# Performance work log

Measured on AMD Instinct MI355X. Metric: run time of the kernel, lower is better.

Reference implementation:

```python
import jax, jax.numpy as jnp
import numpy as np

N_NODES = 50000
N_EDGES = 800000


def _norm(deg):
    # DGL: norm = deg^-0.5 with inf (zero-degree) replaced by 0
    return jnp.where(deg > 0, jax.lax.rsqrt(jnp.maximum(deg, 1.0)), 0.0)


def setup_inputs() -> dict:
    key = jax.random.key(0)
    ks = jax.random.split(key, 8)
    x = jax.random.normal(ks[0], (N_NODES, 128), dtype=jnp.float32)
    W1 = jax.random.normal(ks[1], (128, 128), dtype=jnp.float32) * (1.0 / np.sqrt(128))
    b1 = jnp.zeros((128,), dtype=jnp.float32)
    W2 = jax.random.normal(ks[2], (128, 8), dtype=jnp.float32) * (1.0 / np.sqrt(128))
    b2 = jnp.zeros((8,), dtype=jnp.float32)
    src = jax.random.randint(ks[3], (N_EDGES,), 0, N_NODES, dtype=jnp.int32)
    dst = jax.random.randint(ks[4], (N_EDGES,), 0, N_NODES, dtype=jnp.int32)
    graph_ids = jnp.sort(jax.random.randint(ks[5], (N_NODES,), 0, 100, dtype=jnp.int32))
    return {"x": x, "W1": W1, "b1": b1, "W2": W2, "b2": b2,
            "src": src, "dst": dst, "graph_ids": graph_ids, "num_graphs": 100}


def _graph_conv(x, W, b, src, dst, norm_src, norm_dst):
    # GraphConv norm='both': out = D_in^{-1/2} A (D_out^{-1/2} x W) + b
    h = x @ W                                   # [N, F_out]
    msg = h[src] * norm_src[src, None]          # gather + src norm, [E, F_out]
    agg = jax.ops.segment_sum(msg, dst, num_segments=x.shape[0])  # scatter-add
    return agg * norm_dst[:, None] + b


def reference(x, W1, b1, W2, b2, src, dst, graph_ids, num_graphs):
    n = x.shape[0]
    ones_e = jnp.ones((src.shape[0],), dtype=x.dtype)
    deg_out = jax.ops.segment_sum(ones_e, src, num_segments=n)
    deg_in = jax.ops.segment_sum(ones_e, dst, num_segments=n)
    norm_src = _norm(deg_out)
    norm_dst = _norm(deg_in)

    h = _graph_conv(x, W1, b1, src, dst, norm_src, norm_dst)
    h = jax.nn.relu(h)
    h = _graph_conv(h, W2, b2, src, dst, norm_src, norm_dst)

    # dgl.mean_nodes: per-graph mean of node features
    counts = jax.ops.segment_sum(jnp.ones((n,), dtype=x.dtype), graph_ids,
                                 num_segments=num_graphs)
    sums = jax.ops.segment_sum(h, graph_ids, num_segments=num_graphs)
    return sums / jnp.maximum(counts, 1.0)[:, None]
```

## Files before the change

kernel.cpp:

```cpp
#include <hip/hip_runtime.h>

#define F1 128
#define F2 8
#define CAP 64
#define RH 8192
#define ECH 16384
#define BK 32

typedef unsigned short us8 __attribute__((ext_vector_type(8)));

__device__ inline unsigned short f2bf(float f) {
  unsigned u = __float_as_uint(f);
  u += 0x7FFF + ((u >> 16) & 1);
  return (unsigned short)(u >> 16);
}
__device__ inline float bf2f(unsigned short h) {
  return __uint_as_float(((unsigned)h) << 16);
}

__global__ __launch_bounds__(256) void k_hist(const int* __restrict__ src,
                                              const int* __restrict__ dst,
                                              unsigned short* __restrict__ src16,
                                              unsigned short* __restrict__ dst16,
                                              int* __restrict__ partialA,
                                              int* __restrict__ partialB,
                                              int Epad, int E, int N) {
  __shared__ int binsA[RH];
  __shared__ int binsB[RH];
  int range0 = blockIdx.x * RH;
  int c = blockIdx.y;
  int t = threadIdx.x;
  bool writer = (blockIdx.x == 0);
  for (int i = t; i < RH; i += 256) { binsA[i] = 0; binsB[i] = 0; }
  __syncthreads();
  int e0 = c * ECH, e1 = min(e0 + ECH, Epad);
  for (int base = e0 + t * 4; base < e1; base += 1024) {
    int4 a, b;
    if (base + 4 <= E) {
      a = *(const int4*)&src[base];
      b = *(const int4*)&dst[base];
    } else {
      a.x = (base + 0 < E) ? src[base + 0] : -1;
      a.y = (base + 1 < E) ? src[base + 1] : -1;
      a.z = (base + 2 < E) ? src[base + 2] : -1;
      a.w = (base + 3 < E) ? src[base + 3] : -1;
      b.x = (base + 0 < E) ? dst[base + 0] : -1;
      b.y = (base + 1 < E) ? dst[base + 1] : -1;
      b.z = (base + 2 < E) ? dst[base + 2] : -1;
      b.w = (base + 3 < E) ? dst[base + 3] : -1;
    }
    int av[4] = {a.x, a.y, a.z, a.w};
    int bv[4] = {b.x, b.y, b.z, b.w};
#pragma unroll
    for (int j = 0; j < 4; ++j) {
      int sn = av[j] - range0;
      if (av[j] >= 0 && (unsigned)sn < (unsigned)RH) atomicAdd(&binsA[sn], 1);
      int dn = bv[j] - range0;
      if (bv[j] >= 0 && (unsigned)dn < (unsigned)RH) atomicAdd(&binsB[dn], 1);
    }
    if (writer) {
      ushort4 sa, sb;
      sa.x = av[0] >= 0 ? (unsigned short)av[0] : 0xFFFF;
      sa.y = av[1] >= 0 ? (unsigned short)av[1] : 0xFFFF;
      sa.z = av[2] >= 0 ? (unsigned short)av[2] : 0xFFFF;
      sa.w = av[3] >= 0 ? (unsigned short)av[3] : 0xFFFF;
      sb.x = bv[0] >= 0 ? (unsigned short)bv[0] : 0xFFFF;
      sb.y = bv[1] >= 0 ? (unsigned short)bv[1] : 0xFFFF;
      sb.z = bv[2] >= 0 ? (unsigned short)bv[2] : 0xFFFF;
      sb.w = bv[3] >= 0 ? (unsigned short)bv[3] : 0xFFFF;
      *(ushort4*)&src16[base] = sa;
      *(ushort4*)&dst16[base] = sb;
    }
  }
  __syncthreads();
  for (int i = t; i < RH; i += 256) {
    int n = range0 + i;
    if (n < N) {
      partialA[c * N + n] = binsA[i];
      partialB[c * N + n] = binsB[i];
    }
  }
}

__global__ void k_starts(const int* __restrict__ partialA, const int* __restrict__ partialB,
                         int* __restrict__ starts, int* __restrict__ cnt,
                         float* __restrict__ norm_src, float* __restrict__ norm_dst,
                         unsigned short* __restrict__ esrc16,
                         unsigned short* __restrict__ h1n,
                         float* __restrict__ h2n,
                         float* __restrict__ gsum,
                         const int* __restrict__ gids,
                         float* __restrict__ rcnt,
                         int N, int NCH, int NG) {
  int n = blockIdx.x * 256 + threadIdx.x;
  if (n < NG * F2) gsum[n] = 0.f;
  if (n < NG) {
    int g = n;
    int lo = 0, hi = N;
    while (lo < hi) { int m = (lo + hi) >> 1; if (gids[m] < g) lo = m + 1; else hi = m; }
    int lb = lo;
    lo = 0; hi = N;
    while (lo < hi) { int m = (lo + hi) >> 1; if (gids[m] <= g) lo = m + 1; else hi = m; }
    rcnt[g] = 1.f / fmaxf((float)(lo - lb), 1.f);
  }
  if (n < 16) {
    us8 z = {0, 0, 0, 0, 0, 0, 0, 0};
    *(us8*)&h1n[(size_t)N * 128 + n * 8] = z;
  }
  if (n < 8) h2n[(size_t)N * 8 + n] = 0.f;
  if (n < N) {
    int dout = 0;
#pragma unroll 8
    for (int c = 0; c < NCH; ++c) dout += partialA[c * N + n];
    int run = n * CAP;
#pragma unroll 8
    for (int c = 0; c < NCH; ++c) {
      starts[c * N + n] = run;
      run += partialB[c * N + n];
    }
    int din = run - n * CAP;
    int cn = min(din, CAP);
    cnt[n] = cn;
    int cp = (cn + 15) & ~15;
    for (int pos = cn; pos < cp; ++pos) esrc16[n * CAP + pos] = (unsigned short)N;
    norm_src[n] = dout > 0 ? rsqrtf((float)dout) : 0.f;
    norm_dst[n] = din > 0 ? rsqrtf((float)din) : 0.f;
  }
}

__global__ __launch_bounds__(256) void k_scatter(const unsigned short* __restrict__ src16,
                                                 const unsigned short* __restrict__ dst16,
                                                 const int* __restrict__ starts,
                                                 unsigned short* __restrict__ esrc16,
                                                 int Epad, int N, int NCH) {
  __shared__ int cur[RH];
  int range0 = ((int)blockIdx.x / NCH) * RH;
  int c = (int)blockIdx.x % NCH;
  int t = threadIdx.x;
  for (int i = t; i < RH; i += 256) {
    int n = range0 + i;
    cur[i] = (n < N) ? starts[c * N + n] : 0;
  }
  __syncthreads();
  int e0 = c * ECH, e1 = min(e0 + ECH, Epad);
  for (int base = e0 + t * 8; base < e1; base += 2048) {
    us8 a = *(const us8*)&src16[base];
    us8 b = *(const us8*)&dst16[base];
#pragma unroll
    for (int j = 0; j < 8; ++j) {
      int dn = (int)b[j] - range0;
      if ((unsigned)dn < (unsigned)RH) {
        int node = range0 + dn;
        int p = atomicAdd(&cur[dn], 1);
        if (p < (node + 1) * CAP) esrc16[p] = a[j];
      }
    }
  }
}

__global__ __launch_bounds__(256) void k_gemm1(const float* __restrict__ x,
                                               const float* __restrict__ W1,
                                               const float* __restrict__ norm_src,
                                               unsigned short* __restrict__ h1n, int N) {
  __shared__ float xsT[BK][132];
  __shared__ float Wl[BK][132];
  int row0 = blockIdx.x * 128;
  int tid = threadIdx.x;
  int tc = tid & 15;
  int tr = tid >> 4;
  float acc[8][8] = {{0.f}};

  for (int kb = 0; kb < 128; kb += BK) {
    __syncthreads();
#pragma unroll
    for (int it = 0; it < 4; ++it) {
      int i = tid + it * 256;
      int r = i >> 3, kq = i & 7;
      int grow = row0 + r;
      float4 v = make_float4(0.f, 0.f, 0.f, 0.f);
      if (grow < N) v = *(const float4*)&x[(size_t)grow * 128 + kb + kq * 4];
      xsT[kq * 4 + 0][r] = v.x;
      xsT[kq * 4 + 1][r] = v.y;
      xsT[kq * 4 + 2][r] = v.z;
      xsT[kq * 4 + 3][r] = v.w;
    }
#pragma unroll
    for (int it = 0; it < 4; ++it) {
      int i = tid + it * 256;
      int k = i >> 5, c4 = i & 31;
      *(float4*)&Wl[k][c4 * 4] = *(const float4*)&W1[(size_t)(kb + k) * 128 + c4 * 4];
    }
    __syncthreads();
#pragma unroll 2
    for (int k = 0; k < BK; ++k) {
      float4 xa = *(float4*)&xsT[k][tr * 8];
      float4 xb = *(float4*)&xsT[k][tr * 8 + 4];
      float4 wa = *(float4*)&Wl[k][tc * 4];
      float4 wb = *(float4*)&Wl[k][tc * 4 + 64];
      float xs[8] = {xa.x, xa.y, xa.z, xa.w, xb.x, xb.y, xb.z, xb.w};
      float ws[8] = {wa.x, wa.y, wa.z, wa.w, wb.x, wb.y, wb.z, wb.w};
#pragma unroll
      for (int i = 0; i < 8; ++i)
#pragma unroll
        for (int j = 0; j < 8; ++j) acc[i][j] += xs[i] * ws[j];
    }
  }
#pragma unroll
  for (int i = 0; i < 8; ++i) {
    int grow = row0 + tr * 8 + i;
    if (grow < N) {
      float ns = norm_src[grow];
      ushort4 oa, ob;
      oa.x = f2bf(acc[i][0] * ns); oa.y = f2bf(acc[i][1] * ns);
      oa.z = f2bf(acc[i][2] * ns); oa.w = f2bf(acc[i][3] * ns);
      ob.x = f2bf(acc[i][4] * ns); ob.y = f2bf(acc[i][5] * ns);
      ob.z = f2bf(acc[i][6] * ns); ob.w = f2bf(acc[i][7] * ns);
      *(ushort4*)&h1n[(size_t)grow * 128 + tc * 4] = oa;
      *(ushort4*)&h1n[(size_t)grow * 128 + 64 + tc * 4] = ob;
    }
  }
}

__global__ __launch_bounds__(256) void k_agg1f(const unsigned short* __restrict__ h1n,
                                               const int* __restrict__ cnt,
                                               const unsigned short* __restrict__ esrc16,
                                               const float* __restrict__ norm_dst,
                                               const float* __restrict__ norm_src,
                                               const float* __restrict__ b1,
                                               const float* __restrict__ W2,
                                               float* __restrict__ h2n, int N) {
  int tid = threadIdx.x;
  int lane = tid & 63;
  int g = lane >> 4;
  int fl = lane & 15;
  int node = (blockIdx.x * 256 + tid - lane) / 16 + g;
  if (node >= N) return;
  int cp = (cnt[node] + 15) & ~15;
  int i0 = node * CAP;
  float acc[8] = {0.f, 0.f, 0.f, 0.f, 0.f, 0.f, 0.f, 0.f};
  for (int i = 0; i < cp; i += 16) {
#pragma unroll
    for (int t4 = 0; t4 < 16; t4 += 4) {
      ushort4 ss = *(const ushort4*)&esrc16[i0 + i + t4];
      us8 v0 = *(const us8*)&h1n[(size_t)ss.x * 128 + fl * 8];
      us8 v1 = *(const us8*)&h1n[(size_t)ss.y * 128 + fl * 8];
      us8 v2 = *(const us8*)&h1n[(size_t)ss.z * 128 + fl * 8];
      us8 v3 = *(const us8*)&h1n[(size_t)ss.w * 128 + fl * 8];
#pragma unroll
      for (int j = 0; j < 8; ++j)
        acc[j] += (bf2f(v0[j]) + bf2f(v1[j])) + (bf2f(v2[j]) + bf2f(v3[j]));
    }
  }
  float nd = norm_dst[node];
  float4 bb0 = *(const float4*)&b1[fl * 8];
  float4 bb1 = *(const float4*)&b1[fl * 8 + 4];
  float r[8];
  r[0] = fmaxf(acc[0] * nd + bb0.x, 0.f);
  r[1] = fmaxf(acc[1] * nd + bb0.y, 0.f);
  r[2] = fmaxf(acc[2] * nd + bb0.z, 0.f);
  r[3] = fmaxf(acc[3] * nd + bb0.w, 0.f);
  r[4] = fmaxf(acc[4] * nd + bb1.x, 0.f);
  r[5] = fmaxf(acc[5] * nd + bb1.y, 0.f);
  r[6] = fmaxf(acc[6] * nd + bb1.z, 0.f);
  r[7] = fmaxf(acc[7] * nd + bb1.w, 0.f);
  float4 pa = make_float4(0.f, 0.f, 0.f, 0.f);
  float4 pb = make_float4(0.f, 0.f, 0.f, 0.f);
#pragma unroll
  for (int jj = 0; jj < 8; ++jj) {
    float4 wa = *(const float4*)&W2[(fl * 8 + jj) * 8];
    float4 wb = *(const float4*)&W2[(fl * 8 + jj) * 8 + 4];
    pa.x += r[jj] * wa.x; pa.y += r[jj] * wa.y;
    pa.z += r[jj] * wa.z; pa.w += r[jj] * wa.w;
    pb.x += r[jj] * wb.x; pb.y += r[jj] * wb.y;
    pb.z += r[jj] * wb.z; pb.w += r[jj] * wb.w;
  }
#pragma unroll
  for (int d = 8; d >= 1; d >>= 1) {
    pa.x += __shfl_down(pa.x, d); pa.y += __shfl_down(pa.y, d);
    pa.z += __shfl_down(pa.z, d); pa.w += __shfl_down(pa.w, d);
    pb.x += __shfl_down(pb.x, d); pb.y += __shfl_down(pb.y, d);
    pb.z += __shfl_down(pb.z, d); pb.w += __shfl_down(pb.w, d);
  }
  if (fl == 0) {
    float ns = norm_src[node];
    pa.x *= ns; pa.y *= ns; pa.z *= ns; pa.w *= ns;
    pb.x *= ns; pb.y *= ns; pb.z *= ns; pb.w *= ns;
    *(float4*)&h2n[(size_t)node * 8] = pa;
    *(float4*)&h2n[(size_t)node * 8 + 4] = pb;
  }
}

__global__ __launch_bounds__(256) void k_agg2pool(const float* __restrict__ h2n,
                                                  const int* __restrict__ cnt,
                                                  const unsigned short* __restrict__ esrc16,
                                                  const float* __restrict__ norm_dst,
                                                  const float* __restrict__ b2,
                                                  const int* __restrict__ gids,
                                                  float* __restrict__ gsum, int N) {
  __shared__ float bins[16 * 8];
  __shared__ int sg0;
  int tid = threadIdx.x;
  if (tid < 128) bins[tid] = 0.f;
  int base = blockIdx.x * 32;
  if (tid == 0) sg0 = gids[min(base, N - 1)];
  __syncthreads();
  int node = base + (tid >> 3);
  int j = tid & 7;
  if (node < N) {
    int cp = (cnt[node] + 15) & ~15;
    int i0 = node * CAP;
    float acc = 0.f;
    for (int i = 0; i < cp; i += 8) {
      us8 ss = *(const us8*)&esrc16[i0 + i];
      acc += ((h2n[(size_t)ss[0] * 8 + j] + h2n[(size_t)ss[1] * 8 + j]) +
              (h2n[(size_t)ss[2] * 8 + j] + h2n[(size_t)ss[3] * 8 + j])) +
             ((h2n[(size_t)ss[4] * 8 + j] + h2n[(size_t)ss[5] * 8 + j]) +
              (h2n[(size_t)ss[6] * 8 + j] + h2n[(size_t)ss[7] * 8 + j]));
    }
    float r = acc * norm_dst[node] + b2[j];
    int delta = gids[node] - sg0;
    if (delta < 16) atomicAdd(&bins[delta * 8 + j], r);
    else atomicAdd(&gsum[gids[node] * 8 + j], r);
  }
  __syncthreads();
  if (tid < 128) {
    float v = bins[tid];
    if (v != 0.f) atomicAdd(&gsum[(sg0 + (tid >> 3)) * 8 + (tid & 7)], v);
  }
}

__global__ void k_final(const float* __restrict__ gsum, const float* __restrict__ rcnt,
                        float* __restrict__ out, int total) {
  int i = blockIdx.x * 256 + threadIdx.x;
  if (i < total) out[i] = gsum[i] * rcnt[i >> 3];
}

extern "C" void kernel_launch(void* const* d_in, const int* in_sizes, int n_in,
                              void* d_out, int out_size, void* d_ws, size_t ws_size,
                              hipStream_t stream) {
  const float* x  = (const float*)d_in[0];
  const float* W1 = (const float*)d_in[1];
  const float* b1 = (const float*)d_in[2];
  const float* W2 = (const float*)d_in[3];
  const float* b2 = (const float*)d_in[4];
  const int* src  = (const int*)d_in[5];
  const int* dst  = (const int*)d_in[6];
  const int* gids = (const int*)d_in[7];
  int N = in_sizes[0] / F1;
  int E = in_sizes[5];
  int NG = out_size / F2;
  float* out = (float*)d_out;

  int Epad = (E + 2047) & ~2047;
  int NR  = (N + RH - 1) / RH;
  int NCH = (Epad + ECH - 1) / ECH;

  char* p = (char*)d_ws;
  auto alloc = [&](size_t bytes) -> void* {
    void* r = (void*)p;
    p += (bytes + 255) & ~(size_t)255;
    return r;
  };
  float* gsum    = (float*)alloc((size_t)NG * F2 * 4);
  float* rcnt    = (float*)alloc((size_t)NG * 4);
  unsigned short* src16 = (unsigned short*)alloc((size_t)Epad * 2);
  unsigned short* dst16 = (unsigned short*)alloc((size_t)Epad * 2);
  int* cnt       = (int*)alloc((size_t)N * 4);
  float* norm_src = (float*)alloc((size_t)N * 4);
  float* norm_dst = (float*)alloc((size_t)N * 4);
  unsigned short* esrc16 = (unsigned short*)alloc((size_t)N * CAP * 2);
  unsigned short* h1n = (unsigned short*)alloc((size_t)(N + 1) * F1 * 2);
  float* h2n     = (float*)alloc((size_t)(N + 1) * F2 * 4);
  int* partialA  = (int*)alloc((size_t)NCH * N * 4);
  int* partialB  = (int*)alloc((size_t)NCH * N * 4);
  int* starts    = (int*)alloc((size_t)NCH * N * 4);
  (void)ws_size; (void)n_in;

  k_hist<<<dim3(NR, NCH), 256, 0, stream>>>(src, dst, src16, dst16,
                                            partialA, partialB, Epad, E, N);
  k_starts<<<(N + 255) / 256, 256, 0, stream>>>(partialA, partialB, starts, cnt,
                                                norm_src, norm_dst, esrc16, h1n, h2n,
                                                gsum, gids, rcnt, N, NCH, NG);
  k_scatter<<<NR * NCH, 256, 0, stream>>>(src16, dst16, starts, esrc16, Epad, N, NCH);
  k_gemm1<<<(N + 127) / 128, 256, 0, stream>>>(x, W1, norm_src, h1n, N);
  k_agg1f<<<(N + 15) / 16, 256, 0, stream>>>(h1n, cnt, esrc16, norm_dst, norm_src, b1, W2, h2n, N);
  k_agg2pool<<<((N * 8 + 255) / 256), 256, 0, stream>>>(h2n, cnt, esrc16, norm_dst, b2,
                                                        gids, gsum, N);
  k_final<<<(NG * F2 + 255) / 256, 256, 0, stream>>>(gsum, rcnt, out, NG * F2);
}
```

Baseline: 224.4 us.

## Use split-bf16 MFMA for first GEMM and fold mean scaling into pooling

Replaces the fp32 FMA register-tiled GEMM with bf16 MFMA 16x16x32 instructions. Accuracy is kept by splitting x and W1 into high and low bf16 parts and doing three products per tile. W1 is pre-split and transposed inside k_starts, and x is split on the fly while being staged into shared memory. Separately, the per-graph reciprocal count is applied inside the pooling atomics and the accumulation goes straight into out, which removes the k_final launch and the gsum buffer. The trade-offs are three MFMAs per tile, extra conversion work, and scalar 2-byte output stores in place of vectorized ones.

```diff
diff --git a/kernel.cpp b/kernel.cpp
--- a/kernel.cpp
+++ b/kernel.cpp
@@ -5,9 +5,10 @@
 #define CAP 64
 #define RH 8192
 #define ECH 16384
-#define BK 32
 
 typedef unsigned short us8 __attribute__((ext_vector_type(8)));
+typedef short b16x8 __attribute__((ext_vector_type(8)));
+typedef float f32x4 __attribute__((ext_vector_type(4)));
 
 __device__ inline unsigned short f2bf(float f) {
   unsigned u = __float_as_uint(f);
@@ -88,12 +89,15 @@
                          unsigned short* __restrict__ esrc16,
                          unsigned short* __restrict__ h1n,
                          float* __restrict__ h2n,
-                         float* __restrict__ gsum,
+                         float* __restrict__ out,
                          const int* __restrict__ gids,
                          float* __restrict__ rcnt,
+                         const float* __restrict__ W1,
+                         unsigned short* __restrict__ Wth,
+                         unsigned short* __restrict__ Wtl,
                          int N, int NCH, int NG) {
   int n = blockIdx.x * 256 + threadIdx.x;
-  if (n < NG * F2) gsum[n] = 0.f;
+  if (n < NG * F2) out[n] = 0.f;
   if (n < NG) {
     int g = n;
     int lo = 0, hi = N;
@@ -102,6 +106,14 @@
     lo = 0; hi = N;
     while (lo < hi) { int m = (lo + hi) >> 1; if (gids[m] <= g) lo = m + 1; else hi = m; }
     rcnt[g] = 1.f / fmaxf((float)(lo - lb), 1.f);
+  }
+  if (n < F1 * F1) {
+    int k = n >> 7, cc = n & 127;
+    float v = W1[n];
+    unsigned short hi = f2bf(v);
+    unsigned short lo = f2bf(v - bf2f(hi));
+    Wth[cc * 128 + k] = hi;
+    Wtl[cc * 128 + k] = lo;
   }
   if (n < 16) {
     us8 z = {0, 0, 0, 0, 0, 0, 0, 0};
@@ -159,64 +171,78 @@
 }
 
 __global__ __launch_bounds__(256) void k_gemm1(const float* __restrict__ x,
-                                               const float* __restrict__ W1,
+                                               const unsigned short* __restrict__ Wth,
+                                               const unsigned short* __restrict__ Wtl,
                                                const float* __restrict__ norm_src,
                                                unsigned short* __restrict__ h1n, int N) {
-  __shared__ float xsT[BK][132];
-  __shared__ float Wl[BK][132];
-  int row0 = blockIdx.x * 128;
+  __shared__ unsigned short xh[64][72], xl[64][72];
+  __shared__ unsigned short wh[128][72], wl[128][72];
   int tid = threadIdx.x;
-  int tc = tid & 15;
-  int tr = tid >> 4;
-  float acc[8][8] = {{0.f}};
-
-  for (int kb = 0; kb < 128; kb += BK) {
+  int row0 = blockIdx.x * 64;
+  int L = tid & 63;
+  int wave = tid >> 6;
+  int q = L >> 4, mloc = L & 15;
+  int m0 = wave * 16;
+  f32x4 acc[8];
+#pragma unroll
+  for (int t = 0; t < 8; ++t) acc[t] = (f32x4){0.f, 0.f, 0.f, 0.f};
+
+  for (int kb = 0; kb < 2; ++kb) {
     __syncthreads();
 #pragma unroll
     for (int it = 0; it < 4; ++it) {
-      int i = tid + it * 256;
-      int r = i >> 3, kq = i & 7;
+      int flat = tid + it * 256;
+      int n = flat >> 3, kg = (flat & 7) * 8;
+      us8 vh = *(const us8*)&Wth[n * 128 + kb * 64 + kg];
+      us8 vl = *(const us8*)&Wtl[n * 128 + kb * 64 + kg];
+      *(us8*)&wh[n][kg] = vh;
+      *(us8*)&wl[n][kg] = vl;
+    }
+#pragma unroll
+    for (int it = 0; it < 4; ++it) {
+      int idx = tid + it * 256;
+      int r = idx >> 4, kk = (idx & 15) * 4;
       int grow = row0 + r;
       float4 v = make_float4(0.f, 0.f, 0.f, 0.f);
-      if (grow < N) v = *(const float4*)&x[(size_t)grow * 128 + kb + kq * 4];
-      xsT[kq * 4 + 0][r] = v.x;
-      xsT[kq * 4 + 1][r] = v.y;
-      xsT[kq * 4 + 2][r] = v.z;
-      xsT[kq * 4 + 3][r] = v.w;
-    }
-#pragma unroll
-    for (int it = 0; it < 4; ++it) {
-      int i = tid + it * 256;
-      int k = i >> 5, c4 = i & 31;
-      *(float4*)&Wl[k][c4 * 4] = *(const float4*)&W1[(size_t)(kb + k) * 128 + c4 * 4];
+      if (grow < N) v = *(const float4*)&x[(size_t)grow * 128 + kb * 64 + kk];
+      ushort4 h, l;
+      h.x = f2bf(v.x); l.x = f2bf(v.x - bf2f(h.x));
+      h.y = f2bf(v.y); l.y = f2bf(v.y - bf2f(h.y));
+      h.z = f2bf(v.z); l.z = f2bf(v.z - bf2f(h.z));
+      h.w = f2bf(v.w); l.w = f2bf(v.w - bf2f(h.w));
+      *(ushort4*)&xh[r][kk] = h;
+      *(ushort4*)&xl[r][kk] = l;
     }
     __syncthreads();
-#pragma unroll 2
-    for (int k = 0; k < BK; ++k) {
-      float4 xa = *(float4*)&xsT[k][tr * 8];
-      float4 xb = *(float4*)&xsT[k][tr * 8 + 4];
-      float4 wa = *(float4*)&Wl[k][tc * 4];
-      float4 wb = *(float4*)&Wl[k][tc * 4 + 64];
-      float xs[8] = {xa.x, xa.y, xa.z, xa.w, xb.x, xb.y, xb.z, xb.w};
-      float ws[8] = {wa.x, wa.y, wa.z, wa.w, wb.x, wb.y, wb.z, wb.w};
-#pragma unroll
-      for (int i = 0; i < 8; ++i)
-#pragma unroll
-        for (int j = 0; j < 8; ++j) acc[i][j] += xs[i] * ws[j];
-    }
-  }
-#pragma unroll
-  for (int i = 0; i < 8; ++i) {
-    int grow = row0 + tr * 8 + i;
-    if (grow < N) {
-      float ns = norm_src[grow];
-      ushort4 oa, ob;
-      oa.x = f2bf(acc[i][0] * ns); oa.y = f2bf(acc[i][1] * ns);
-      oa.z = f2bf(acc[i][2] * ns); oa.w = f2bf(acc[i][3] * ns);
-      ob.x = f2bf(acc[i][4] * ns); ob.y = f2bf(acc[i][5] * ns);
-      ob.z = f2bf(acc[i][6] * ns); ob.w = f2bf(acc[i][7] * ns);
-      *(ushort4*)&h1n[(size_t)grow * 128 + tc * 4] = oa;
-      *(ushort4*)&h1n[(size_t)grow * 128 + 64 + tc * 4] = ob;
+#pragma unroll
+    for (int ks = 0; ks < 2; ++ks) {
+      int koff = ks * 32 + q * 8;
+      b16x8 ah = *(const b16x8*)&xh[m0 + mloc][koff];
+      b16x8 al = *(const b16x8*)&xl[m0 + mloc][koff];
+#pragma unroll
+      for (int t = 0; t < 8; ++t) {
+        b16x8 bh = *(const b16x8*)&wh[t * 16 + mloc][koff];
+        b16x8 bl = *(const b16x8*)&wl[t * 16 + mloc][koff];
+        acc[t] = __builtin_amdgcn_mfma_f32_16x16x32_bf16(ah, bh, acc[t], 0, 0, 0);
+        acc[t] = __builtin_amdgcn_mfma_f32_16x16x32_bf16(ah, bl, acc[t], 0, 0, 0);
+        acc[t] = __builtin_amdgcn_mfma_f32_16x16x32_bf16(al, bh, acc[t], 0, 0, 0);
+      }
+    }
+  }
+  int rows[4];
+  float ns[4];
+#pragma unroll
+  for (int reg = 0; reg < 4; ++reg) {
+    rows[reg] = row0 + m0 + q * 4 + reg;
+    ns[reg] = (rows[reg] < N) ? norm_src[rows[reg]] : 0.f;
+  }
+#pragma unroll
+  for (int t = 0; t < 8; ++t) {
+    int col = t * 16 + mloc;
+#pragma unroll
+    for (int reg = 0; reg < 4; ++reg) {
+      if (rows[reg] < N)
+        h1n[(size_t)rows[reg] * 128 + col] = f2bf(acc[t][reg] * ns[reg]);
     }
   }
 }
@@ -296,7 +322,8 @@
                                                   const float* __restrict__ norm_dst,
                                                   const float* __restrict__ b2,
                                                   const int* __restrict__ gids,
-                                                  float* __restrict__ gsum, int N) {
+                                                  const float* __restrict__ rcnt,
+                                                  float* __restrict__ out, int N) {
   __shared__ float bins[16 * 8];
   __shared__ int sg0;
   int tid = threadIdx.x;
@@ -318,21 +345,19 @@
               (h2n[(size_t)ss[6] * 8 + j] + h2n[(size_t)ss[7] * 8 + j]));
     }
     float r = acc * norm_dst[node] + b2[j];
-    int delta = gids[node] - sg0;
+    int gid = gids[node];
+    int delta = gid - sg0;
     if (delta < 16) atomicAdd(&bins[delta * 8 + j], r);
-    else atomicAdd(&gsum[gids[node] * 8 + j], r);
+    else atomicAdd(&out[gid * 8 + j], r * rcnt[gid]);
   }
   __syncthreads();
   if (tid < 128) {
     float v = bins[tid];
-    if (v != 0.f) atomicAdd(&gsum[(sg0 + (tid >> 3)) * 8 + (tid & 7)], v);
-  }
-}
-
-__global__ void k_final(const float* __restrict__ gsum, const float* __restrict__ rcnt,
-                        float* __restrict__ out, int total) {
-  int i = blockIdx.x * 256 + threadIdx.x;
-  if (i < total) out[i] = gsum[i] * rcnt[i >> 3];
+    if (v != 0.f) {
+      int gq = sg0 + (tid >> 3);
+      atomicAdd(&out[gq * 8 + (tid & 7)], v * rcnt[gq]);
+    }
+  }
 }
 
 extern "C" void kernel_launch(void* const* d_in, const int* in_sizes, int n_in,
@@ -361,7 +386,6 @@
     p += (bytes + 255) & ~(size_t)255;
     return r;
   };
-  float* gsum    = (float*)alloc((size_t)NG * F2 * 4);
   float* rcnt    = (float*)alloc((size_t)NG * 4);
   unsigned short* src16 = (unsigned short*)alloc((size_t)Epad * 2);
   unsigned short* dst16 = (unsigned short*)alloc((size_t)Epad * 2);
@@ -371,6 +395,8 @@
   unsigned short* esrc16 = (unsigned short*)alloc((size_t)N * CAP * 2);
   unsigned short* h1n = (unsigned short*)alloc((size_t)(N + 1) * F1 * 2);
   float* h2n     = (float*)alloc((size_t)(N + 1) * F2 * 4);
+  unsigned short* Wth = (unsigned short*)alloc((size_t)F1 * F1 * 2);
+  unsigned short* Wtl = (unsigned short*)alloc((size_t)F1 * F1 * 2);
   int* partialA  = (int*)alloc((size_t)NCH * N * 4);
   int* partialB  = (int*)alloc((size_t)NCH * N * 4);
   int* starts    = (int*)alloc((size_t)NCH * N * 4);
@@ -380,11 +406,10 @@
                                             partialA, partialB, Epad, E, N);
   k_starts<<<(N + 255) / 256, 256, 0, stream>>>(partialA, partialB, starts, cnt,
                                                 norm_src, norm_dst, esrc16, h1n, h2n,
-                                                gsum, gids, rcnt, N, NCH, NG);
+                                                out, gids, rcnt, W1, Wth, Wtl, N, NCH, NG);
   k_scatter<<<NR * NCH, 256, 0, stream>>>(src16, dst16, starts, esrc16, Epad, N, NCH);
-  k_gemm1<<<(N + 127) / 128, 256, 0, stream>>>(x, W1, norm_src, h1n, N);
+  k_gemm1<<<(N + 63) / 64, 256, 0, stream>>>(x, Wth, Wtl, norm_src, h1n, N);
   k_agg1f<<<(N + 15) / 16, 256, 0, stream>>>(h1n, cnt, esrc16, norm_dst, norm_src, b1, W2, h2n, N);
   k_agg2pool<<<((N * 8 + 255) / 256), 256, 0, stream>>>(h2n, cnt, esrc16, norm_dst, b2,
-                                                        gids, gsum, N);
-  k_final<<<(NG * F2 + 255) / 256, 256, 0, stream>>>(gsum, rcnt, out, NG * F2);
-}
+                                                        gids, rcnt, out, N);
+}
```

Result: faster. 217.1 us (-3.3%).
